# Performance work log

Hardware: AMD Instinct MI355X
Metric: run time of the kernel (lower is better)

## Reference

```python
import jax, jax.numpy as jnp
import numpy as np

N_NODES = 100000
N_EDGES = 1600000
NUM_GRAPHS = 1000
NODE_IN, EDGE_IN = 32, 16
NODE_EMB, EDGE_EMB, HID, OUT, L = 64, 32, 64, 1, 3
EPS = 1e-5


def _glorot(key, shape):
    fan_in = shape[0]
    return jax.random.normal(key, shape, jnp.float32) / np.sqrt(fan_in)


def setup_inputs() -> dict:
    key = jax.random.key(0)
    ks = jax.random.split(key, 16)
    inp = {
        "x": jax.random.normal(ks[0], (N_NODES, NODE_IN), jnp.float32),
        "edge_attr": jax.random.normal(ks[1], (N_EDGES, EDGE_IN), jnp.float32),
        "edge_index": jax.random.randint(ks[2], (2, N_EDGES), 0, N_NODES, jnp.int64
                                         if jax.config.jax_enable_x64 else jnp.int32),
        "batch": jnp.sort(jax.random.randint(ks[3], (N_NODES,), 0, NUM_GRAPHS)),
        # embeddings
        "node_W": _glorot(ks[4], (NODE_IN, NODE_EMB)),
        "node_b": jnp.zeros((NODE_EMB,), jnp.float32),
        "edge_W": _glorot(ks[5], (EDGE_IN, EDGE_EMB)),
        "edge_b": jnp.zeros((EDGE_EMB,), jnp.float32),
        # per-layer MPNN params (node_dim==64 for every layer since node_emb_dim==hidden_dim)
        "msg_W": _glorot(ks[6], (L, NODE_EMB + EDGE_EMB, HID)),
        "msg_b": jnp.zeros((L, HID), jnp.float32),
        "msg_gamma": jnp.ones((L, HID), jnp.float32),
        "msg_beta": jnp.zeros((L, HID), jnp.float32),
        "upd_W": _glorot(ks[7], (L, NODE_EMB + HID, HID)),
        "upd_b": jnp.zeros((L, HID), jnp.float32),
        "upd_gamma": jnp.ones((L, HID), jnp.float32),
        "upd_beta": jnp.zeros((L, HID), jnp.float32),
        # readout
        "r1_W": _glorot(ks[8], (HID, HID)),
        "r1_b": jnp.zeros((HID,), jnp.float32),
        "r2_W": _glorot(ks[9], (HID, OUT)),
        "r2_b": jnp.zeros((OUT,), jnp.float32),
    }
    return inp


def _bn(h, gamma, beta):
    # BatchNorm1d in training mode: normalize with batch mean / biased variance
    mu = jnp.mean(h, axis=0)
    var = jnp.mean(jnp.square(h - mu), axis=0)
    return gamma * (h - mu) * jax.lax.rsqrt(var + EPS) + beta


def reference(x, edge_attr, edge_index, batch,
              node_W, node_b, edge_W, edge_b,
              msg_W, msg_b, msg_gamma, msg_beta,
              upd_W, upd_b, upd_gamma, upd_beta,
              r1_W, r1_b, r2_W, r2_b):
    h = x @ node_W + node_b                       # [N, 64]
    e = edge_attr @ edge_W + edge_b               # [E, 32]
    src, dst = edge_index[0], edge_index[1]
    for i in range(L):
        # message: gather x_j, concat edge feats, Linear-ReLU-BN (dropout = eval/no-op)
        m = jnp.concatenate([h[src], e], axis=-1) @ msg_W[i] + msg_b[i]   # [E, 64]
        m = _bn(jax.nn.relu(m), msg_gamma[i], msg_beta[i])
        # aggregate: scatter-add to destination nodes
        agg = jax.ops.segment_sum(m, dst, num_segments=N_NODES)          # [N, 64]
        # update: concat self feats, Linear-ReLU-BN
        u = jnp.concatenate([h, agg], axis=-1) @ upd_W[i] + upd_b[i]     # [N, 64]
        h = _bn(jax.nn.relu(u), upd_gamma[i], upd_beta[i])
    # global add pool over graphs
    g = jax.ops.segment_sum(h, batch, num_segments=NUM_GRAPHS)           # [G, 64]
    out = jax.nn.relu(g @ r1_W + r1_b) @ r2_W + r2_b                     # [G, 1]
    return out
```

## Files before the change

kernel.cpp:

```cpp
#include <hip/hip_runtime.h>
#include <hip/hip_bf16.h>

#define N_NODES   100000
#define N_EDGES   1600000
#define NUM_GRAPHS 1000

typedef unsigned int u32;
typedef unsigned short u16;

typedef __bf16 bf16_t;
typedef bf16_t bf16x8 __attribute__((ext_vector_type(8)));
typedef float  f32x4  __attribute__((ext_vector_type(4)));

__device__ __forceinline__ float bf2f(u16 u){ return __uint_as_float(((u32)u)<<16); }
__device__ __forceinline__ float BL(u32 u){ return __uint_as_float(u<<16); }
__device__ __forceinline__ float BH(u32 u){ return __uint_as_float(u&0xffff0000u); }
__device__ __forceinline__ u16 f2bf(float f){
  u32 u = __float_as_uint(f);
  return (u16)((u + 0x7fffu + ((u>>16)&1u)) >> 16);
}
__device__ __forceinline__ float ldf(const void* p, size_t i, int isbf){
  return isbf ? bf2f(((const u16*)p)[i]) : ((const float*)p)[i];
}

union U4BF { uint4 u; bf16x8 v; };

__global__ void k_detect(const u32* __restrict__ x, int* __restrict__ flag){
  int t = threadIdx.x; int cnt = 0;
  for (int i = t; i < 256; i += 64){
    u32 w = x[i];
    u32 e = (w >> 7) & 0xffu;
    if (e >= 110u && e <= 137u) cnt++;
  }
  for (int o = 32; o; o >>= 1) cnt += __shfl_xor(cnt, o);
  if (t == 0) *flag = (cnt > 128) ? 1 : 0;
}

__global__ void k_prep(const void* __restrict__ eW, const void* __restrict__ eb,
                       const void* __restrict__ mW, const void* __restrict__ mb,
                       u16* __restrict__ Wcol, u16* __restrict__ Weff,
                       float* __restrict__ uaff, const int* __restrict__ flagp){
  int isbf = *flagp;
  int l = blockIdx.x, c = threadIdx.x;
  u16* W = Wcol + ((size_t)l*64 + c)*96;
  for (int k = 0; k < 64; k++)
    W[k] = f2bf(ldf(mW, (size_t)(l*96 + k)*64 + c, isbf));
  for (int j = 0; j < 16; j++){
    float acc = 0.f;
    for (int k = 0; k < 32; k++)
      acc += ldf(eW, (size_t)j*32 + k, isbf) * ldf(mW, (size_t)(l*96 + 64 + k)*64 + c, isbf);
    W[64 + j] = f2bf(acc);
  }
  float fbv = ldf(mb, (size_t)l*64 + c, isbf);
  for (int k = 0; k < 32; k++)
    fbv += ldf(eb, k, isbf) * ldf(mW, (size_t)(l*96 + 64 + k)*64 + c, isbf);
  W[80] = f2bf(fbv);
  for (int k = 81; k < 96; k++) W[k] = 0;
  if (l == 0){
    u16* We = Weff + (size_t)c*96;
    for (int k = 0; k < 96; k++) We[k] = W[k];
    uaff[c] = 1.0f; uaff[64 + c] = 0.0f;
  }
}

__global__ void k_fold(const u16* __restrict__ Wcol, u16* __restrict__ Weff,
                       const float* __restrict__ uaff, int lnext){
  int c = threadIdx.x;
  const u16* src = Wcol + ((size_t)lnext*64 + c)*96;
  u16* dst = Weff + ((size_t)lnext*64 + c)*96;
  float bias = bf2f(src[80]);
  for (int k = 0; k < 64; k++){
    float w = bf2f(src[k]);
    dst[k] = f2bf(w * uaff[k]);
    bias = fmaf(uaff[64 + k], w, bias);
  }
  for (int k = 64; k < 80; k++) dst[k] = src[k];
  dst[80] = f2bf(bias);
  for (int k = 81; k < 96; k++) dst[k] = 0;
}

__global__ void k_node_emb(const void* __restrict__ x, const void* __restrict__ nW,
                           const void* __restrict__ nb, float* __restrict__ h,
                           u16* __restrict__ h_bf, const int* __restrict__ flagp){
  int isbf = *flagp;
  int lane = threadIdx.x & 63;
  int gw = (blockIdx.x*blockDim.x + threadIdx.x) >> 6;
  int nw = (gridDim.x*blockDim.x) >> 6;
  float w[32];
#pragma unroll
  for (int k = 0; k < 32; k++) w[k] = ldf(nW, (size_t)k*64 + lane, isbf);
  float bias = ldf(nb, lane, isbf);
  for (int n = gw; n < N_NODES; n += nw){
    float acc = bias;
    if (isbf){
      const uint4* xr = (const uint4*)((const u16*)x + (size_t)n*32);
#pragma unroll
      for (int q = 0; q < 4; q++){
        uint4 a = xr[q];
        u32 uu[4] = {a.x, a.y, a.z, a.w};
#pragma unroll
        for (int j = 0; j < 4; j++){
          acc = fmaf(BL(uu[j]), w[q*8 + 2*j + 0], acc);
          acc = fmaf(BH(uu[j]), w[q*8 + 2*j + 1], acc);
        }
      }
    } else {
      const float4* xr = (const float4*)((const float*)x + (size_t)n*32);
#pragma unroll
      for (int q = 0; q < 8; q++){
        float4 a = xr[q];
        acc = fmaf(a.x, w[q*4+0], acc); acc = fmaf(a.y, w[q*4+1], acc);
        acc = fmaf(a.z, w[q*4+2], acc); acc = fmaf(a.w, w[q*4+3], acc);
      }
    }
    h[(size_t)n*64 + lane] = acc;
    h_bf[(size_t)n*64 + lane] = f2bf(acc);
  }
}

__global__ void k_deg(const int* __restrict__ ei, int* __restrict__ deg){
  int i = blockIdx.x*blockDim.x + threadIdx.x;
  int stride = gridDim.x*blockDim.x;
  for (int e = i; e < N_EDGES; e += stride)
    atomicAdd(&deg[ei[N_EDGES + e]], 1);
}

__global__ void __launch_bounds__(256) k_scan1(const int* __restrict__ deg,
                                               int* __restrict__ bsum){
  __shared__ int wsum[4];
  int b = blockIdx.x, t = threadIdx.x;
  int i0 = b*512 + t;
  int s = 0;
  if (i0 < N_NODES) s += deg[i0];
  if (i0 + 256 < N_NODES) s += deg[i0 + 256];
  for (int o = 32; o; o >>= 1) s += __shfl_xor(s, o);
  if ((t & 63) == 0) wsum[t >> 6] = s;
  __syncthreads();
  if (t == 0) bsum[b] = wsum[0] + wsum[1] + wsum[2] + wsum[3];
}

__global__ void k_scan2(const int* __restrict__ bsum, int* __restrict__ boff,
                        int* __restrict__ rp){
  __shared__ int l[200];
  int t = threadIdx.x;
  if (t < 196) l[t] = bsum[t];
  __syncthreads();
  if (t == 0){
    int r = 0;
    for (int k = 0; k < 196; k++){ int x = l[k]; l[k] = r; r += x; }
    rp[N_NODES] = r;
  }
  __syncthreads();
  if (t < 196) boff[t] = l[t];
}

__global__ void __launch_bounds__(256) k_scan3(const int* __restrict__ deg,
                        const int* __restrict__ boff, int* __restrict__ rp,
                        int* __restrict__ cursor, float* __restrict__ degf){
  __shared__ int wpre[4];
  int b = blockIdx.x, t = threadIdx.x;
  int i0 = b*512 + 2*t;
  int d0 = (i0     < N_NODES) ? deg[i0]     : 0;
  int d1 = (i0 + 1 < N_NODES) ? deg[i0 + 1] : 0;
  int s = d0 + d1;
  int incl = s;
  for (int o = 1; o < 64; o <<= 1){ int u = __shfl_up(incl, o); if ((t & 63) >= o) incl += u; }
  if ((t & 63) == 63) wpre[t >> 6] = incl;
  __syncthreads();
  if (t == 0){ int r = 0; for (int k = 0; k < 4; k++){ int x = wpre[k]; wpre[k] = r; r += x; } }
  __syncthreads();
  int excl = boff[b] + wpre[t >> 6] + incl - s;
  if (i0 < N_NODES){
    rp[i0] = excl; cursor[i0] = excl; degf[i0] = (float)d0;
  }
  if (i0 + 1 < N_NODES){
    rp[i0+1] = excl + d0; cursor[i0+1] = excl + d0; degf[i0+1] = (float)d1;
  }
}

__global__ void k_scatter(const int* __restrict__ ei, int* __restrict__ cursor,
                          int* __restrict__ perm2){
  int i = blockIdx.x*blockDim.x + threadIdx.x;
  int stride = gridDim.x*blockDim.x;
  for (int e = i; e < N_EDGES; e += stride){
    int d = ei[N_EDGES + e];
    int p = atomicAdd(&cursor[d], 1);
    ((int2*)perm2)[p] = make_int2(ei[e], e);
  }
}

__global__ void __launch_bounds__(256) k_msgmm(
    const u16* __restrict__ h_bf, const void* __restrict__ ea,
    const int* __restrict__ rp, const int* __restrict__ perm2,
    const u16* __restrict__ Weff, float* __restrict__ agg,
    float* __restrict__ stats, const int* __restrict__ flagp,
    int l, int nwaves){
  __shared__ float bs[128];
  int tid = threadIdx.x;
  if (tid < 128) bs[tid] = 0.f;
  __syncthreads();
  int isbf = *flagp;
  int lane = tid & 63, wv = tid >> 6;
  int w = blockIdx.x*4 + wv;
  long long t0 = (long long)w     * N_EDGES / nwaves;
  long long t1 = (long long)(w+1) * N_EDGES / nwaves;
  int lo = 0, hi = N_NODES;
  while (lo < hi){ int mid = (lo+hi)>>1; if ((long long)rp[mid] < t0) lo = mid+1; else hi = mid; }
  int n0 = lo, n1;
  if (w == nwaves-1) n1 = N_NODES;
  else {
    lo = 0; hi = N_NODES;
    while (lo < hi){ int mid = (lo+hi)>>1; if ((long long)rp[mid] < t1) lo = mid+1; else hi = mid; }
    n1 = lo;
  }
  int nn = lane & 15, kg = lane >> 4;
  bf16x8 B[3][4];
  const u16* Wl = Weff + (size_t)l*64*96;
#pragma unroll
  for (int t = 0; t < 4; t++)
#pragma unroll
    for (int kb = 0; kb < 3; kb++)
      B[kb][t] = *(const bf16x8*)(Wl + (size_t)(t*16+nn)*96 + kb*32 + kg*8);
  U4BF ac; ac.u = make_uint4((kg==2)? 0x3f80u : 0u, 0u, 0u, 0u);
  float s1[4] = {0,0,0,0}, s2[4] = {0,0,0,0};
  for (int n = n0; n < n1; n++){
    int b0 = rp[n], b1 = rp[n+1];
    float r0 = 0.f, r1 = 0.f, r2 = 0.f, r3 = 0.f;
    for (int base = b0; base < b1; base += 16){
      int rem = b1 - base; if (rem > 16) rem = 16;
      int row = (nn < rem) ? nn : rem-1;
      int2 p = ((const int2*)perm2)[base + row];
      const uint4* hp = (const uint4*)(h_bf + (size_t)p.x*64);
      U4BF fA, fB, fC;
      fA.u = hp[kg];
      fB.u = hp[4 + kg];
      if (kg < 2){
        if (isbf){
          fC.u = ((const uint4*)ea)[(size_t)p.y*2 + kg];
        } else {
          const float4* ef = (const float4*)ea;
          float4 f0 = ef[(size_t)p.y*4 + kg*2];
          float4 f1 = ef[(size_t)p.y*4 + kg*2 + 1];
          fC.u.x = (u32)f2bf(f0.x) | ((u32)f2bf(f0.y)<<16);
          fC.u.y = (u32)f2bf(f0.z) | ((u32)f2bf(f0.w)<<16);
          fC.u.z = (u32)f2bf(f1.x) | ((u32)f2bf(f1.y)<<16);
          fC.u.w = (u32)f2bf(f1.z) | ((u32)f2bf(f1.w)<<16);
        }
      } else fC = ac;
      f32x4 a0 = {0,0,0,0}, a1 = {0,0,0,0}, a2 = {0,0,0,0}, a3 = {0,0,0,0};
      a0 = __builtin_amdgcn_mfma_f32_16x16x32_bf16(fA.v, B[0][0], a0, 0,0,0);
      a1 = __builtin_amdgcn_mfma_f32_16x16x32_bf16(fA.v, B[0][1], a1, 0,0,0);
      a2 = __builtin_amdgcn_mfma_f32_16x16x32_bf16(fA.v, B[0][2], a2, 0,0,0);
      a3 = __builtin_amdgcn_mfma_f32_16x16x32_bf16(fA.v, B[0][3], a3, 0,0,0);
      a0 = __builtin_amdgcn_mfma_f32_16x16x32_bf16(fB.v, B[1][0], a0, 0,0,0);
      a1 = __builtin_amdgcn_mfma_f32_16x16x32_bf16(fB.v, B[1][1], a1, 0,0,0);
      a2 = __builtin_amdgcn_mfma_f32_16x16x32_bf16(fB.v, B[1][2], a2, 0,0,0);
      a3 = __builtin_amdgcn_mfma_f32_16x16x32_bf16(fB.v, B[1][3], a3, 0,0,0);
      a0 = __builtin_amdgcn_mfma_f32_16x16x32_bf16(fC.v, B[2][0], a0, 0,0,0);
      a1 = __builtin_amdgcn_mfma_f32_16x16x32_bf16(fC.v, B[2][1], a1, 0,0,0);
      a2 = __builtin_amdgcn_mfma_f32_16x16x32_bf16(fC.v, B[2][2], a2, 0,0,0);
      a3 = __builtin_amdgcn_mfma_f32_16x16x32_bf16(fC.v, B[2][3], a3, 0,0,0);
      int rowbase = kg*4;
      float ts0 = 0.f, ts1 = 0.f, ts2 = 0.f, ts3 = 0.f;
#pragma unroll
      for (int j = 0; j < 4; j++){
        bool valid = (rowbase + j) < rem;
        float m0 = fmaxf(a0[j], 0.f); m0 = valid ? m0 : 0.f;
        float m1 = fmaxf(a1[j], 0.f); m1 = valid ? m1 : 0.f;
        float m2 = fmaxf(a2[j], 0.f); m2 = valid ? m2 : 0.f;
        float m3 = fmaxf(a3[j], 0.f); m3 = valid ? m3 : 0.f;
        ts0 += m0; ts1 += m1; ts2 += m2; ts3 += m3;
        s2[0] = fmaf(m0,m0,s2[0]); s2[1] = fmaf(m1,m1,s2[1]);
        s2[2] = fmaf(m2,m2,s2[2]); s2[3] = fmaf(m3,m3,s2[3]);
      }
      s1[0] += ts0; s1[1] += ts1; s1[2] += ts2; s1[3] += ts3;
      ts0 += __shfl_xor(ts0,16); ts0 += __shfl_xor(ts0,32);
      ts1 += __shfl_xor(ts1,16); ts1 += __shfl_xor(ts1,32);
      ts2 += __shfl_xor(ts2,16); ts2 += __shfl_xor(ts2,32);
      ts3 += __shfl_xor(ts3,16); ts3 += __shfl_xor(ts3,32);
      r0 += ts0; r1 += ts1; r2 += ts2; r3 += ts3;
    }
    float v = (kg==0) ? r0 : (kg==1) ? r1 : (kg==2) ? r2 : r3;
    agg[(size_t)n*64 + lane] = v;
  }
#pragma unroll
  for (int t = 0; t < 4; t++){
    atomicAdd(&bs[t*16+nn], s1[t]);
    atomicAdd(&bs[64+t*16+nn], s2[t]);
  }
  __syncthreads();
  if (tid < 128) atomicAdd(&stats[tid], bs[tid]);
}

__global__ void k_fin(float* __restrict__ stats, const void* __restrict__ gamma,
                      const void* __restrict__ beta, float* __restrict__ aff,
                      float cnt_inv, int goff, const int* __restrict__ flagp){
  int isbf = *flagp; int c = threadIdx.x;
  float mu  = stats[c]      * cnt_inv;
  float var = stats[64 + c] * cnt_inv - mu*mu;
  float rs  = rsqrtf(var + 1e-5f);
  float g = ldf(gamma, (size_t)goff + c, isbf);
  float b = ldf(beta,  (size_t)goff + c, isbf);
  aff[c]      = g*rs;
  aff[64 + c] = b - g*mu*rs;
  stats[c] = 0.f; stats[64 + c] = 0.f;
}

__global__ void __launch_bounds__(256) k_upd(
    float* __restrict__ h, u16* __restrict__ h_bf, const float* __restrict__ agg,
    const float* __restrict__ degf, const float* __restrict__ maff,
    const float* __restrict__ aff_prev,
    const void* __restrict__ uW, const void* __restrict__ ub,
    float* __restrict__ stats, const int* __restrict__ flagp, int l){
  __shared__ float bs[128];
  if (threadIdx.x < 128) bs[threadIdx.x] = 0.f;
  __syncthreads();
  int isbf = *flagp;
  int lane = threadIdx.x & 63;
  int gw = (blockIdx.x*blockDim.x + threadIdx.x) >> 6;
  int nw = (gridDim.x*blockDim.x) >> 6;
  float wa[64], wb[64]; float tv = 0.f, tv2 = 0.f;
#pragma unroll
  for (int k = 0; k < 64; k++){
    float wka = ldf(uW, (size_t)(l*128 + k)*64 + lane, isbf);
    wa[k] = wka * aff_prev[k];
    tv2 = fmaf(aff_prev[64 + k], wka, tv2);
    float wk = ldf(uW, (size_t)(l*128 + 64 + k)*64 + lane, isbf);
    wb[k] = wk * maff[k];
    tv = fmaf(maff[64 + k], wk, tv);
  }
  float bias = ldf(ub, (size_t)l*64 + lane, isbf) + tv2;
  float s1 = 0.f, s2 = 0.f;
  for (int n = gw; n < N_NODES; n += nw){
    const float4* hr = (const float4*)(h + (size_t)n*64);
    const float4* ar = (const float4*)(agg + (size_t)n*64);
    float a0 = fmaf(degf[n], tv, bias), a1 = 0.f, a2 = 0.f, a3 = 0.f;
#pragma unroll
    for (int q = 0; q < 8; q++){
      float4 a = hr[2*q+0];
      a0 = fmaf(a.x, wa[8*q+0], a0); a0 = fmaf(a.y, wa[8*q+1], a0);
      a0 = fmaf(a.z, wa[8*q+2], a0); a0 = fmaf(a.w, wa[8*q+3], a0);
      float4 b = hr[2*q+1];
      a1 = fmaf(b.x, wa[8*q+4], a1); a1 = fmaf(b.y, wa[8*q+5], a1);
      a1 = fmaf(b.z, wa[8*q+6], a1); a1 = fmaf(b.w, wa[8*q+7], a1);
      float4 c = ar[2*q+0];
      a2 = fmaf(c.x, wb[8*q+0], a2); a2 = fmaf(c.y, wb[8*q+1], a2);
      a2 = fmaf(c.z, wb[8*q+2], a2); a2 = fmaf(c.w, wb[8*q+3], a2);
      float4 d = ar[2*q+1];
      a3 = fmaf(d.x, wb[8*q+4], a3); a3 = fmaf(d.y, wb[8*q+5], a3);
      a3 = fmaf(d.z, wb[8*q+6], a3); a3 = fmaf(d.w, wb[8*q+7], a3);
    }
    float rl = fmaxf((a0 + a1) + (a2 + a3), 0.f);
    h[(size_t)n*64 + lane] = rl;
    h_bf[(size_t)n*64 + lane] = f2bf(rl);
    s1 += rl;
    s2 = fmaf(rl, rl, s2);
  }
  atomicAdd(&bs[lane], s1);
  atomicAdd(&bs[64 + lane], s2);
  __syncthreads();
  if (threadIdx.x < 128) atomicAdd(&stats[threadIdx.x], bs[threadIdx.x]);
}

__global__ void k_pool(const float* __restrict__ h, const int* __restrict__ batch,
                       const float* __restrict__ uaff, float* __restrict__ g){
  int lane = threadIdx.x & 63;
  int gw = (blockIdx.x*blockDim.x + threadIdx.x) >> 6;
  int nw = (gridDim.x*blockDim.x) >> 6;
  float s = uaff[lane], t = uaff[64 + lane];
  int chunk = (N_NODES + nw - 1) / nw;
  int n0 = gw*chunk;
  int n1 = n0 + chunk; if (n1 > N_NODES) n1 = N_NODES;
  int cur = -1; float acc = 0.f;
  for (int n = n0; n < n1; n++){
    int b = batch[n];
    float v = fmaf(s, h[(size_t)n*64 + lane], t);
    if (b != cur){
      if (cur >= 0) atomicAdd(&g[(size_t)cur*64 + lane], acc);
      cur = b; acc = v;
    } else acc += v;
  }
  if (cur >= 0) atomicAdd(&g[(size_t)cur*64 + lane], acc);
}

__global__ void k_read(const float* __restrict__ g, const void* __restrict__ r1W,
                       const void* __restrict__ r1b, const void* __restrict__ r2W,
                       const void* __restrict__ r2b, void* __restrict__ out,
                       const int* __restrict__ flagp){
  int isbf = *flagp;
  int lane = threadIdx.x;
  int gr = blockIdx.x;
  float w[64];
#pragma unroll
  for (int k = 0; k < 64; k++) w[k] = ldf(r1W, (size_t)k*64 + lane, isbf);
  float acc = ldf(r1b, lane, isbf);
  const float4* grow = (const float4*)(g + (size_t)gr*64);
#pragma unroll
  for (int q = 0; q < 16; q++){
    float4 a = grow[q];
    acc = fmaf(a.x, w[4*q+0], acc); acc = fmaf(a.y, w[4*q+1], acc);
    acc = fmaf(a.z, w[4*q+2], acc); acc = fmaf(a.w, w[4*q+3], acc);
  }
  float hid = fmaxf(acc, 0.f);
  float p = hid * ldf(r2W, lane, isbf);
  for (int o = 32; o; o >>= 1) p += __shfl_xor(p, o);
  if (lane == 0){
    float v = p + ldf(r2b, 0, isbf);
    if (isbf) ((__hip_bfloat16*)out)[gr] = __float2bfloat16(v);
    else      ((float*)out)[gr] = v;
  }
}

extern "C" void kernel_launch(void* const* d_in, const int* in_sizes, int n_in,
                              void* d_out, int out_size, void* d_ws, size_t ws_size,
                              hipStream_t stream){
  const void* x    = d_in[0];
  const void* ea   = d_in[1];
  const int*  ei   = (const int*)d_in[2];
  const int*  bt   = (const int*)d_in[3];
  const void* nW   = d_in[4];  const void* nb  = d_in[5];
  const void* eW   = d_in[6];  const void* eb  = d_in[7];
  const void* mW   = d_in[8];  const void* mb  = d_in[9];
  const void* mg   = d_in[10]; const void* mbe = d_in[11];
  const void* uW   = d_in[12]; const void* ub  = d_in[13];
  const void* ug   = d_in[14]; const void* ube = d_in[15];
  const void* r1W  = d_in[16]; const void* r1b = d_in[17];
  const void* r2W  = d_in[18]; const void* r2b = d_in[19];

  float* ws = (float*)d_ws;
  float* h        = ws + 0;
  float* agg      = ws + 6400000;
  u16*   h_bf     = (u16*)(ws + 12800000);
  int*   perm2    = (int*)(ws + 16000000);
  float* degf     = ws + 19200000;
  int*   deg_i    = (int*)(ws + 19300000);
  float* g        = ws + 19400000;
  float* mstats   = ws + 19464000;
  float* ustats   = ws + 19464128;
  float* maff     = ws + 19464256;
  float* uaff     = ws + 19464384;
  int*   flag     = (int*)(ws + 19464512);
  u16*   Wcol     = (u16*)(ws + 19464528);
  u16*   Weff     = (u16*)(ws + 19473744);
  int*   row_ptr  = (int*)(ws + 19482960);
  int*   cursor   = (int*)(ws + 19582964);
  int*   bsum     = (int*)(ws + 19682964);
  int*   boff     = (int*)(ws + 19683160);

  const int MM_BLOCKS = 2048;
  const int MM_WAVES  = MM_BLOCKS * 4;

  k_detect<<<1, 64, 0, stream>>>((const u32*)x, flag);
  hipMemsetAsync(ws + 19300000, 0, 164256*sizeof(float), stream);
  k_prep<<<3, 64, 0, stream>>>(eW, eb, mW, mb, Wcol, Weff, uaff, flag);
  k_node_emb<<<256, 256, 0, stream>>>(x, nW, nb, h, h_bf, flag);
  k_deg<<<512, 256, 0, stream>>>(ei, deg_i);
  k_scan1<<<196, 256, 0, stream>>>(deg_i, bsum);
  k_scan2<<<1, 256, 0, stream>>>(bsum, boff, row_ptr);
  k_scan3<<<196, 256, 0, stream>>>(deg_i, boff, row_ptr, cursor, degf);
  k_scatter<<<512, 256, 0, stream>>>(ei, cursor, perm2);

  for (int l = 0; l < 3; l++){
    k_msgmm<<<MM_BLOCKS, 256, 0, stream>>>(h_bf, ea, row_ptr, perm2, Weff,
                                           agg, mstats, flag, l, MM_WAVES);
    k_fin<<<1, 64, 0, stream>>>(mstats, mg, mbe, maff, 1.0f/(float)N_EDGES, l*64, flag);
    k_upd<<<1024, 256, 0, stream>>>(h, h_bf, agg, degf, maff, uaff, uW, ub,
                                    ustats, flag, l);
    k_fin<<<1, 64, 0, stream>>>(ustats, ug, ube, uaff, 1.0f/(float)N_NODES, l*64, flag);
    if (l < 2) k_fold<<<1, 64, 0, stream>>>(Wcol, Weff, uaff, l+1);
  }

  k_pool<<<128, 256, 0, stream>>>(h, bt, uaff, g);
  k_read<<<NUM_GRAPHS, 64, 0, stream>>>(g, r1W, r1b, r2W, r2b, d_out, flag);
}
```

Measured before the change: 1.581 ms.

## Use split-bf16 MFMA for node update and apply BN in a separate normalize pass

The scalar FP32 per-lane update GEMM is replaced with an MFMA kernel that takes hi/lo bf16 split inputs to keep near-fp32 accuracy. Node and aggregate buffers are stored as split bf16 pairs instead of fp32 plus bf16 copies. Folding the previous layer's BN into the next message weights is replaced by a separate k_norm pass that writes normalized h explicitly. This adds an extra node-sized pass and extra MFMAs for the lo parts, in exchange for cheaper update compute.

```diff
diff --git a/kernel.cpp b/kernel.cpp
--- a/kernel.cpp
+++ b/kernel.cpp
@@ -38,11 +38,10 @@
 
 __global__ void k_prep(const void* __restrict__ eW, const void* __restrict__ eb,
                        const void* __restrict__ mW, const void* __restrict__ mb,
-                       u16* __restrict__ Wcol, u16* __restrict__ Weff,
-                       float* __restrict__ uaff, const int* __restrict__ flagp){
+                       u16* __restrict__ Weff, const int* __restrict__ flagp){
   int isbf = *flagp;
   int l = blockIdx.x, c = threadIdx.x;
-  u16* W = Wcol + ((size_t)l*64 + c)*96;
+  u16* W = Weff + ((size_t)l*64 + c)*96;
   for (int k = 0; k < 64; k++)
     W[k] = f2bf(ldf(mW, (size_t)(l*96 + k)*64 + c, isbf));
   for (int j = 0; j < 16; j++){
@@ -56,32 +55,32 @@
     fbv += ldf(eb, k, isbf) * ldf(mW, (size_t)(l*96 + 64 + k)*64 + c, isbf);
   W[80] = f2bf(fbv);
   for (int k = 81; k < 96; k++) W[k] = 0;
-  if (l == 0){
-    u16* We = Weff + (size_t)c*96;
-    for (int k = 0; k < 96; k++) We[k] = W[k];
-    uaff[c] = 1.0f; uaff[64 + c] = 0.0f;
-  }
-}
-
-__global__ void k_fold(const u16* __restrict__ Wcol, u16* __restrict__ Weff,
-                       const float* __restrict__ uaff, int lnext){
-  int c = threadIdx.x;
-  const u16* src = Wcol + ((size_t)lnext*64 + c)*96;
-  u16* dst = Weff + ((size_t)lnext*64 + c)*96;
-  float bias = bf2f(src[80]);
+}
+
+__global__ void k_updprep(const void* __restrict__ uW, const void* __restrict__ ub,
+                          const float* __restrict__ maff,
+                          u16* __restrict__ Wupd, float* __restrict__ biasv,
+                          float* __restrict__ tvv, const int* __restrict__ flagp, int l){
+  int isbf = *flagp; int c = threadIdx.x;
+  u16* W = Wupd + (size_t)c*192;
+  float tv = 0.f;
   for (int k = 0; k < 64; k++){
-    float w = bf2f(src[k]);
-    dst[k] = f2bf(w * uaff[k]);
-    bias = fmaf(uaff[64 + k], w, bias);
-  }
-  for (int k = 64; k < 80; k++) dst[k] = src[k];
-  dst[80] = f2bf(bias);
-  for (int k = 81; k < 96; k++) dst[k] = 0;
+    float wka = ldf(uW, (size_t)(l*128 + k)*64 + c, isbf);
+    W[k] = f2bf(wka);
+    float wkb = ldf(uW, (size_t)(l*128 + 64 + k)*64 + c, isbf);
+    float prod = wkb * maff[k];
+    u16 hi = f2bf(prod);
+    W[64 + k]  = hi;
+    W[128 + k] = f2bf(prod - bf2f(hi));
+    tv = fmaf(maff[64 + k], wkb, tv);
+  }
+  biasv[c] = ldf(ub, (size_t)l*64 + c, isbf);
+  tvv[c] = tv;
 }
 
 __global__ void k_node_emb(const void* __restrict__ x, const void* __restrict__ nW,
-                           const void* __restrict__ nb, float* __restrict__ h,
-                           u16* __restrict__ h_bf, const int* __restrict__ flagp){
+                           const void* __restrict__ nb, u16* __restrict__ hsp,
+                           const int* __restrict__ flagp){
   int isbf = *flagp;
   int lane = threadIdx.x & 63;
   int gw = (blockIdx.x*blockDim.x + threadIdx.x) >> 6;
@@ -113,8 +112,9 @@
         acc = fmaf(a.z, w[q*4+2], acc); acc = fmaf(a.w, w[q*4+3], acc);
       }
     }
-    h[(size_t)n*64 + lane] = acc;
-    h_bf[(size_t)n*64 + lane] = f2bf(acc);
+    u16 hi = f2bf(acc);
+    hsp[(size_t)n*128 + lane]      = hi;
+    hsp[(size_t)n*128 + 64 + lane] = f2bf(acc - bf2f(hi));
   }
 }
 
@@ -190,9 +190,9 @@
 }
 
 __global__ void __launch_bounds__(256) k_msgmm(
-    const u16* __restrict__ h_bf, const void* __restrict__ ea,
+    const u16* __restrict__ hsp, const void* __restrict__ ea,
     const int* __restrict__ rp, const int* __restrict__ perm2,
-    const u16* __restrict__ Weff, float* __restrict__ agg,
+    const u16* __restrict__ Weff, u16* __restrict__ aggs,
     float* __restrict__ stats, const int* __restrict__ flagp,
     int l, int nwaves){
   __shared__ float bs[128];
@@ -230,7 +230,7 @@
       int rem = b1 - base; if (rem > 16) rem = 16;
       int row = (nn < rem) ? nn : rem-1;
       int2 p = ((const int2*)perm2)[base + row];
-      const uint4* hp = (const uint4*)(h_bf + (size_t)p.x*64);
+      const uint4* hp = (const uint4*)(hsp + (size_t)p.x*128);
       U4BF fA, fB, fC;
       fA.u = hp[kg];
       fB.u = hp[4 + kg];
@@ -281,7 +281,9 @@
       r0 += ts0; r1 += ts1; r2 += ts2; r3 += ts3;
     }
     float v = (kg==0) ? r0 : (kg==1) ? r1 : (kg==2) ? r2 : r3;
-    agg[(size_t)n*64 + lane] = v;
+    u16 hiv = f2bf(v);
+    aggs[(size_t)n*128 + lane]      = hiv;
+    aggs[(size_t)n*128 + 64 + lane] = f2bf(v - bf2f(hiv));
   }
 #pragma unroll
   for (int t = 0; t < 4; t++){
@@ -306,75 +308,107 @@
   stats[c] = 0.f; stats[64 + c] = 0.f;
 }
 
-__global__ void __launch_bounds__(256) k_upd(
-    float* __restrict__ h, u16* __restrict__ h_bf, const float* __restrict__ agg,
-    const float* __restrict__ degf, const float* __restrict__ maff,
-    const float* __restrict__ aff_prev,
-    const void* __restrict__ uW, const void* __restrict__ ub,
-    float* __restrict__ stats, const int* __restrict__ flagp, int l){
+#define UPD_TILES (N_NODES/16)
+__global__ void __launch_bounds__(256) k_updmm(
+    const u16* __restrict__ hsp, u16* __restrict__ aggs,
+    const float* __restrict__ degf, const u16* __restrict__ Wupd,
+    const float* __restrict__ biasv, const float* __restrict__ tvv,
+    float* __restrict__ stats){
   __shared__ float bs[128];
-  if (threadIdx.x < 128) bs[threadIdx.x] = 0.f;
-  __syncthreads();
-  int isbf = *flagp;
-  int lane = threadIdx.x & 63;
-  int gw = (blockIdx.x*blockDim.x + threadIdx.x) >> 6;
-  int nw = (gridDim.x*blockDim.x) >> 6;
-  float wa[64], wb[64]; float tv = 0.f, tv2 = 0.f;
-#pragma unroll
-  for (int k = 0; k < 64; k++){
-    float wka = ldf(uW, (size_t)(l*128 + k)*64 + lane, isbf);
-    wa[k] = wka * aff_prev[k];
-    tv2 = fmaf(aff_prev[64 + k], wka, tv2);
-    float wk = ldf(uW, (size_t)(l*128 + 64 + k)*64 + lane, isbf);
-    wb[k] = wk * maff[k];
-    tv = fmaf(maff[64 + k], wk, tv);
-  }
-  float bias = ldf(ub, (size_t)l*64 + lane, isbf) + tv2;
-  float s1 = 0.f, s2 = 0.f;
-  for (int n = gw; n < N_NODES; n += nw){
-    const float4* hr = (const float4*)(h + (size_t)n*64);
-    const float4* ar = (const float4*)(agg + (size_t)n*64);
-    float a0 = fmaf(degf[n], tv, bias), a1 = 0.f, a2 = 0.f, a3 = 0.f;
-#pragma unroll
-    for (int q = 0; q < 8; q++){
-      float4 a = hr[2*q+0];
-      a0 = fmaf(a.x, wa[8*q+0], a0); a0 = fmaf(a.y, wa[8*q+1], a0);
-      a0 = fmaf(a.z, wa[8*q+2], a0); a0 = fmaf(a.w, wa[8*q+3], a0);
-      float4 b = hr[2*q+1];
-      a1 = fmaf(b.x, wa[8*q+4], a1); a1 = fmaf(b.y, wa[8*q+5], a1);
-      a1 = fmaf(b.z, wa[8*q+6], a1); a1 = fmaf(b.w, wa[8*q+7], a1);
-      float4 c = ar[2*q+0];
-      a2 = fmaf(c.x, wb[8*q+0], a2); a2 = fmaf(c.y, wb[8*q+1], a2);
-      a2 = fmaf(c.z, wb[8*q+2], a2); a2 = fmaf(c.w, wb[8*q+3], a2);
-      float4 d = ar[2*q+1];
-      a3 = fmaf(d.x, wb[8*q+4], a3); a3 = fmaf(d.y, wb[8*q+5], a3);
-      a3 = fmaf(d.z, wb[8*q+6], a3); a3 = fmaf(d.w, wb[8*q+7], a3);
+  int tid = threadIdx.x;
+  if (tid < 128) bs[tid] = 0.f;
+  __syncthreads();
+  int lane = tid & 63;
+  int nn = lane & 15, kg = lane >> 4;
+  int w = blockIdx.x*4 + (tid >> 6);
+  int nwv = gridDim.x*4;
+  bf16x8 B[6][4];
+#pragma unroll
+  for (int t = 0; t < 4; t++)
+#pragma unroll
+    for (int kb = 0; kb < 6; kb++)
+      B[kb][t] = *(const bf16x8*)(Wupd + (size_t)(t*16+nn)*192 + kb*32 + kg*8);
+  float bc[4], tc[4];
+#pragma unroll
+  for (int t = 0; t < 4; t++){ bc[t] = biasv[t*16+nn]; tc[t] = tvv[t*16+nn]; }
+  float s1[4] = {0,0,0,0}, s2[4] = {0,0,0,0};
+  for (int tile = w; tile < UPD_TILES; tile += nwv){
+    int n0 = tile*16;
+    int r = n0 + nn;
+    const uint4* hp = (const uint4*)hsp;
+    const uint4* ap = (const uint4*)aggs;
+    U4BF hh0, hh1, hl0, hl1, ah0, ah1, al0, al1;
+    hh0.u = hp[(size_t)r*16 + kg];       hh1.u = hp[(size_t)r*16 + 4 + kg];
+    hl0.u = hp[(size_t)r*16 + 8 + kg];   hl1.u = hp[(size_t)r*16 + 12 + kg];
+    ah0.u = ap[(size_t)r*16 + kg];       ah1.u = ap[(size_t)r*16 + 4 + kg];
+    al0.u = ap[(size_t)r*16 + 8 + kg];   al1.u = ap[(size_t)r*16 + 12 + kg];
+    float dg[4];
+#pragma unroll
+    for (int j = 0; j < 4; j++) dg[j] = degf[n0 + kg*4 + j];
+    f32x4 a0 = {0,0,0,0}, a1 = {0,0,0,0}, a2 = {0,0,0,0}, a3 = {0,0,0,0};
+#define MF(F,KB) \
+    a0 = __builtin_amdgcn_mfma_f32_16x16x32_bf16(F.v, B[KB][0], a0, 0,0,0); \
+    a1 = __builtin_amdgcn_mfma_f32_16x16x32_bf16(F.v, B[KB][1], a1, 0,0,0); \
+    a2 = __builtin_amdgcn_mfma_f32_16x16x32_bf16(F.v, B[KB][2], a2, 0,0,0); \
+    a3 = __builtin_amdgcn_mfma_f32_16x16x32_bf16(F.v, B[KB][3], a3, 0,0,0);
+    MF(hh0,0) MF(hh1,1) MF(hl0,0) MF(hl1,1)
+    MF(ah0,2) MF(ah1,3) MF(ah0,4) MF(ah1,5)
+    MF(al0,2) MF(al1,3)
+#undef MF
+#pragma unroll
+    for (int j = 0; j < 4; j++){
+      int n = n0 + kg*4 + j;
+      float m0 = fmaxf(fmaf(tc[0], dg[j], a0[j] + bc[0]), 0.f);
+      float m1 = fmaxf(fmaf(tc[1], dg[j], a1[j] + bc[1]), 0.f);
+      float m2 = fmaxf(fmaf(tc[2], dg[j], a2[j] + bc[2]), 0.f);
+      float m3 = fmaxf(fmaf(tc[3], dg[j], a3[j] + bc[3]), 0.f);
+      s1[0] += m0; s1[1] += m1; s1[2] += m2; s1[3] += m3;
+      s2[0] = fmaf(m0,m0,s2[0]); s2[1] = fmaf(m1,m1,s2[1]);
+      s2[2] = fmaf(m2,m2,s2[2]); s2[3] = fmaf(m3,m3,s2[3]);
+      u16* hw = aggs + (size_t)n*128;
+      u16 q0 = f2bf(m0), q1 = f2bf(m1), q2 = f2bf(m2), q3 = f2bf(m3);
+      hw[     nn] = q0;  hw[64 +      nn] = f2bf(m0 - bf2f(q0));
+      hw[16 + nn] = q1;  hw[64 + 16 + nn] = f2bf(m1 - bf2f(q1));
+      hw[32 + nn] = q2;  hw[64 + 32 + nn] = f2bf(m2 - bf2f(q2));
+      hw[48 + nn] = q3;  hw[64 + 48 + nn] = f2bf(m3 - bf2f(q3));
     }
-    float rl = fmaxf((a0 + a1) + (a2 + a3), 0.f);
-    h[(size_t)n*64 + lane] = rl;
-    h_bf[(size_t)n*64 + lane] = f2bf(rl);
-    s1 += rl;
-    s2 = fmaf(rl, rl, s2);
-  }
-  atomicAdd(&bs[lane], s1);
-  atomicAdd(&bs[64 + lane], s2);
-  __syncthreads();
-  if (threadIdx.x < 128) atomicAdd(&stats[threadIdx.x], bs[threadIdx.x]);
-}
-
-__global__ void k_pool(const float* __restrict__ h, const int* __restrict__ batch,
-                       const float* __restrict__ uaff, float* __restrict__ g){
+  }
+#pragma unroll
+  for (int t = 0; t < 4; t++){
+    atomicAdd(&bs[t*16+nn], s1[t]);
+    atomicAdd(&bs[64+t*16+nn], s2[t]);
+  }
+  __syncthreads();
+  if (tid < 128) atomicAdd(&stats[tid], bs[tid]);
+}
+
+__global__ void k_norm(const u16* __restrict__ aggs, const float* __restrict__ uaff,
+                       u16* __restrict__ hsp){
   int lane = threadIdx.x & 63;
   int gw = (blockIdx.x*blockDim.x + threadIdx.x) >> 6;
   int nw = (gridDim.x*blockDim.x) >> 6;
   float s = uaff[lane], t = uaff[64 + lane];
+  for (int n = gw; n < N_NODES; n += nw){
+    float v = bf2f(aggs[(size_t)n*128 + lane]) + bf2f(aggs[(size_t)n*128 + 64 + lane]);
+    float o = fmaf(s, v, t);
+    u16 hi = f2bf(o);
+    hsp[(size_t)n*128 + lane]      = hi;
+    hsp[(size_t)n*128 + 64 + lane] = f2bf(o - bf2f(hi));
+  }
+}
+
+__global__ void k_pool(const u16* __restrict__ hsp, const int* __restrict__ batch,
+                       float* __restrict__ g){
+  int lane = threadIdx.x & 63;
+  int gw = (blockIdx.x*blockDim.x + threadIdx.x) >> 6;
+  int nw = (gridDim.x*blockDim.x) >> 6;
   int chunk = (N_NODES + nw - 1) / nw;
   int n0 = gw*chunk;
   int n1 = n0 + chunk; if (n1 > N_NODES) n1 = N_NODES;
   int cur = -1; float acc = 0.f;
   for (int n = n0; n < n1; n++){
     int b = batch[n];
-    float v = fmaf(s, h[(size_t)n*64 + lane], t);
+    float v = bf2f(hsp[(size_t)n*128 + lane]) + bf2f(hsp[(size_t)n*128 + 64 + lane]);
     if (b != cur){
       if (cur >= 0) atomicAdd(&g[(size_t)cur*64 + lane], acc);
       cur = b; acc = v;
@@ -428,32 +462,34 @@
   const void* r2W  = d_in[18]; const void* r2b = d_in[19];
 
   float* ws = (float*)d_ws;
-  float* h        = ws + 0;
-  float* agg      = ws + 6400000;
-  u16*   h_bf     = (u16*)(ws + 12800000);
-  int*   perm2    = (int*)(ws + 16000000);
-  float* degf     = ws + 19200000;
-  int*   deg_i    = (int*)(ws + 19300000);
-  float* g        = ws + 19400000;
-  float* mstats   = ws + 19464000;
-  float* ustats   = ws + 19464128;
-  float* maff     = ws + 19464256;
-  float* uaff     = ws + 19464384;
-  int*   flag     = (int*)(ws + 19464512);
-  u16*   Wcol     = (u16*)(ws + 19464528);
-  u16*   Weff     = (u16*)(ws + 19473744);
-  int*   row_ptr  = (int*)(ws + 19482960);
-  int*   cursor   = (int*)(ws + 19582964);
-  int*   bsum     = (int*)(ws + 19682964);
-  int*   boff     = (int*)(ws + 19683160);
+  u16*   hsp      = (u16*)(ws + 0);
+  u16*   aggs     = (u16*)(ws + 6400000);
+  int*   perm2    = (int*)(ws + 12800000);
+  float* degf     = ws + 16000000;
+  int*   deg_i    = (int*)(ws + 16100000);
+  float* g        = ws + 16200000;
+  float* mstats   = ws + 16264000;
+  float* ustats   = ws + 16264128;
+  float* maff     = ws + 16264256;
+  float* uaff     = ws + 16264384;
+  int*   flag     = (int*)(ws + 16264512);
+  u16*   Weff     = (u16*)(ws + 16264528);
+  u16*   Wupd     = (u16*)(ws + 16273744);
+  float* biasv    = ws + 16279888;
+  float* tvv      = ws + 16279952;
+  int*   row_ptr  = (int*)(ws + 16280016);
+  int*   cursor   = (int*)(ws + 16380020);
+  int*   bsum     = (int*)(ws + 16480020);
+  int*   boff     = (int*)(ws + 16480216);
 
   const int MM_BLOCKS = 2048;
   const int MM_WAVES  = MM_BLOCKS * 4;
+  const int UPD_BLOCKS = 782;
 
   k_detect<<<1, 64, 0, stream>>>((const u32*)x, flag);
-  hipMemsetAsync(ws + 19300000, 0, 164256*sizeof(float), stream);
-  k_prep<<<3, 64, 0, stream>>>(eW, eb, mW, mb, Wcol, Weff, uaff, flag);
-  k_node_emb<<<256, 256, 0, stream>>>(x, nW, nb, h, h_bf, flag);
+  hipMemsetAsync(ws + 16100000, 0, 164256*sizeof(float), stream);
+  k_prep<<<3, 64, 0, stream>>>(eW, eb, mW, mb, Weff, flag);
+  k_node_emb<<<256, 256, 0, stream>>>(x, nW, nb, hsp, flag);
   k_deg<<<512, 256, 0, stream>>>(ei, deg_i);
   k_scan1<<<196, 256, 0, stream>>>(deg_i, bsum);
   k_scan2<<<1, 256, 0, stream>>>(bsum, boff, row_ptr);
@@ -461,15 +497,16 @@
   k_scatter<<<512, 256, 0, stream>>>(ei, cursor, perm2);
 
   for (int l = 0; l < 3; l++){
-    k_msgmm<<<MM_BLOCKS, 256, 0, stream>>>(h_bf, ea, row_ptr, perm2, Weff,
-                                           agg, mstats, flag, l, MM_WAVES);
+    k_msgmm<<<MM_BLOCKS, 256, 0, stream>>>(hsp, ea, row_ptr, perm2, Weff,
+                                           aggs, mstats, flag, l, MM_WAVES);
     k_fin<<<1, 64, 0, stream>>>(mstats, mg, mbe, maff, 1.0f/(float)N_EDGES, l*64, flag);
-    k_upd<<<1024, 256, 0, stream>>>(h, h_bf, agg, degf, maff, uaff, uW, ub,
-                                    ustats, flag, l);
+    k_updprep<<<1, 64, 0, stream>>>(uW, ub, maff, Wupd, biasv, tvv, flag, l);
+    k_updmm<<<UPD_BLOCKS, 256, 0, stream>>>(hsp, aggs, degf, Wupd, biasv, tvv,
+                                            ustats);
     k_fin<<<1, 64, 0, stream>>>(ustats, ug, ube, uaff, 1.0f/(float)N_NODES, l*64, flag);
-    if (l < 2) k_fold<<<1, 64, 0, stream>>>(Wcol, Weff, uaff, l+1);
-  }
-
-  k_pool<<<128, 256, 0, stream>>>(h, bt, uaff, g);
+    k_norm<<<256, 256, 0, stream>>>(aggs, uaff, hsp);
+  }
+
+  k_pool<<<128, 256, 0, stream>>>(hsp, bt, g);
   k_read<<<NUM_GRAPHS, 64, 0, stream>>>(g, r1W, r1b, r2W, r2b, d_out, flag);
 }
```

Result: faster. 1.455 ms (-8.0%).
